# Kernel tuning notes

Hardware: AMD Instinct MI355X
Metric: run time of the kernel (lower is better)

## Reference

```python
import jax, jax.numpy as jnp
import numpy as np

N, D, R = 65536, 32, 128


def setup_inputs() -> dict:
    key = jax.random.key(0)
    k1, k2, k3, k4 = jax.random.split(key, 4)
    X = jax.random.normal(k1, (N, D), dtype=jnp.float32)
    a = jax.random.normal(k2, (R, D), dtype=jnp.float32)
    b = jax.random.uniform(k3, (R, D), dtype=jnp.float32)  # positive, like abs(randn)
    c = jax.random.normal(k4, (R, D + 1), dtype=jnp.float32)
    return {"X": X, "a": a, "b": b, "c": c}


def reference(X, a, b, c):
    # Gaussian membership per (sample, rule, dim): exp(-(x-a)^2 / (2*clamp(b,1e-8)^2))
    b_cl = jnp.clip(b, 1e-8)                      # [R, D]
    diff = X[:, None, :] - a[None, :, :]          # [N, R, D]
    mu = jnp.exp(-(diff * diff) / (2.0 * b_cl * b_cl))
    strengths = jnp.prod(mu, axis=2)              # [N, R] rule firing strengths
    strengths_sum = jnp.sum(strengths, axis=1, keepdims=True)
    normalized = strengths / (strengths_sum + 1e-8)
    # consequent: linear model per rule, X @ c[:, :-1].T + bias
    rule_out = X @ c[:, :-1].T + c[:, -1]         # [N, R]
    predictions = jnp.sum(normalized * rule_out, axis=1)  # [N]
    return (predictions, strengths, normalized)
```

## Files before the change

kernel.cpp:

```cpp
#include <hip/hip_runtime.h>

#define NS 65536
#define DD 32
#define RR 128
#define SPB 16
#define STR 132

__global__ __launch_bounds__(128, 4) void anfis_main(
    const float* __restrict__ X, const float* __restrict__ A,
    const float* __restrict__ B, const float* __restrict__ C,
    float* __restrict__ out_pred, float* __restrict__ out_str,
    float* __restrict__ out_norm)
{
    __shared__ float SBUF[SPB * STR];
    __shared__ float PBUF[SPB * STR];
    __shared__ float pS[SPB][8];
    __shared__ float pD[SPB][8];
    __shared__ float scale_lds[SPB];

    const int tid   = threadIdx.x;
    const int nbase = blockIdx.x * SPB;

    float w_[DD], naw_[DD], ck_[DD], bias;
    {
        const float4* av = (const float4*)(A + tid * DD);
        const float4* bv = (const float4*)(B + tid * DD);
        #pragma unroll
        for (int i = 0; i < 8; ++i) {
            float4 va = av[i], vb = bv[i];
            float w0 = 0.8493218003f * __builtin_amdgcn_rcpf(fmaxf(vb.x, 1e-8f));
            float w1 = 0.8493218003f * __builtin_amdgcn_rcpf(fmaxf(vb.y, 1e-8f));
            float w2 = 0.8493218003f * __builtin_amdgcn_rcpf(fmaxf(vb.z, 1e-8f));
            float w3 = 0.8493218003f * __builtin_amdgcn_rcpf(fmaxf(vb.w, 1e-8f));
            w_[4*i+0] = w0; naw_[4*i+0] = -va.x * w0;
            w_[4*i+1] = w1; naw_[4*i+1] = -va.y * w1;
            w_[4*i+2] = w2; naw_[4*i+2] = -va.z * w2;
            w_[4*i+3] = w3; naw_[4*i+3] = -va.w * w3;
        }
        #pragma unroll
        for (int d = 0; d < DD; ++d) ck_[d] = C[tid * (DD + 1) + d];
        bias = C[tid * (DD + 1) + DD];
    }

    const float* Xg = X + (size_t)nbase * DD;

    float xa[DD], xb[DD];
#define LOADX(arr, jj) { _Pragma("unroll") \
    for (int i = 0; i < DD; ++i) arr[i] = Xg[(jj) * DD + i]; }

#define COMPUTE(arr, jj) { \
    float s0 = 0.f, s1 = 0.f, s2 = 0.f, s3 = 0.f; \
    float r0 = bias, r1 = 0.f, r2 = 0.f, r3 = 0.f; \
    _Pragma("unroll") \
    for (int d = 0; d < DD; d += 4) { \
        float t0 = fmaf(arr[d+0], w_[d+0], naw_[d+0]); s0 = fmaf(t0, t0, s0); r0 = fmaf(arr[d+0], ck_[d+0], r0); \
        float t1 = fmaf(arr[d+1], w_[d+1], naw_[d+1]); s1 = fmaf(t1, t1, s1); r1 = fmaf(arr[d+1], ck_[d+1], r1); \
        float t2 = fmaf(arr[d+2], w_[d+2], naw_[d+2]); s2 = fmaf(t2, t2, s2); r2 = fmaf(arr[d+2], ck_[d+2], r2); \
        float t3 = fmaf(arr[d+3], w_[d+3], naw_[d+3]); s3 = fmaf(t3, t3, s3); r3 = fmaf(arr[d+3], ck_[d+3], r3); \
    } \
    float st = __builtin_amdgcn_exp2f(-((s0 + s1) + (s2 + s3))); \
    float ro = (r0 + r1) + (r2 + r3); \
    SBUF[(jj) * STR + tid] = st; \
    PBUF[(jj) * STR + tid] = st * ro; }

    LOADX(xa, 0)
    for (int j = 0; j < SPB; j += 2) {
        LOADX(xb, j + 1)
        COMPUTE(xa, j)
        if (j + 2 < SPB) LOADX(xa, j + 2)
        COMPUTE(xb, j + 1)
    }
#undef LOADX
#undef COMPUTE
    __syncthreads();

    {
        int s = tid >> 3, o = tid & 7;
        const float4* srow = (const float4*)&SBUF[s * STR + o * 16];
        const float4* prow = (const float4*)&PBUF[s * STR + o * 16];
        float ss = 0.f, dd = 0.f;
        #pragma unroll
        for (int k = 0; k < 4; ++k) {
            float4 v = srow[k]; ss += (v.x + v.y) + (v.z + v.w);
            float4 p = prow[k]; dd += (p.x + p.y) + (p.z + p.w);
        }
        pS[s][o] = ss; pD[s][o] = dd;
    }
    __syncthreads();
    if (tid < SPB) {
        float ss = 0.f, dd = 0.f;
        #pragma unroll
        for (int o = 0; o < 8; ++o) { ss += pS[tid][o]; dd += pD[tid][o]; }
        float sc = 1.0f / (ss + 1e-8f);
        out_pred[nbase + tid] = dd * sc;
        scale_lds[tid] = sc;
    }
    __syncthreads();

    #pragma unroll
    for (int it = 0; it < 4; ++it) {
        int f   = it * 128 + tid;
        int row = f >> 5;
        int col = f & 31;
        float4 v = *(const float4*)&SBUF[row * STR + col * 4];
        float sc = scale_lds[row];
        size_t base = ((size_t)(nbase + row)) * RR + col * 4;
        *(float4*)(out_str  + base) = v;
        *(float4*)(out_norm + base) = make_float4(v.x * sc, v.y * sc, v.z * sc, v.w * sc);
    }
}

extern "C" void kernel_launch(void* const* d_in, const int* in_sizes, int n_in,
                              void* d_out, int out_size, void* d_ws, size_t ws_size,
                              hipStream_t stream) {
    const float* X = (const float*)d_in[0];
    const float* A = (const float*)d_in[1];
    const float* B = (const float*)d_in[2];
    const float* C = (const float*)d_in[3];

    float* pred = (float*)d_out;
    float* str  = pred + NS;
    float* nrm  = str + (size_t)NS * RR;

    anfis_main<<<dim3(NS / SPB), dim3(128), 0, stream>>>(X, A, B, C, pred, str, nrm);
}
```

Before: 107.8 us.

## Process eight sample tiles per block with LDS-staged parameters and deferred stores

Each block now loops over eight 16-sample tiles instead of handling one. The per-rule weights, offsets and consequent coefficients are moved from registers into swizzled LDS arrays, and the loop is reordered so each thread accumulates 16 samples in registers while reading the block-uniform X rows. The strength and normalized outputs of the previous tile are written during the next tile's iteration, so global stores can overlap with compute; these stores are now per-thread scalar stores instead of float4 ones. This aims to spread parameter setup over more samples and hide store latency, at the cost of a lower occupancy target (launch bounds 2), more LDS use, and extra per-tile synchronisation.

```diff
diff --git a/kernel.cpp b/kernel.cpp
--- a/kernel.cpp
+++ b/kernel.cpp
@@ -3,110 +3,143 @@
 #define NS 65536
 #define DD 32
 #define RR 128
-#define SPB 16
-#define STR 132
+#define SPT 16
+#define TPB 8
+#define NBLK (NS / (SPT * TPB))
+#define TSTR 132
 
-__global__ __launch_bounds__(128, 4) void anfis_main(
+__global__ __launch_bounds__(128, 2) void anfis_main(
     const float* __restrict__ X, const float* __restrict__ A,
     const float* __restrict__ B, const float* __restrict__ C,
     float* __restrict__ out_pred, float* __restrict__ out_str,
     float* __restrict__ out_norm)
 {
-    __shared__ float SBUF[SPB * STR];
-    __shared__ float PBUF[SPB * STR];
-    __shared__ float pS[SPB][8];
-    __shared__ float pD[SPB][8];
-    __shared__ float scale_lds[SPB];
+    __shared__ float PW[RR * DD];
+    __shared__ float PN[RR * DD];
+    __shared__ float PK[RR * DD];
+    __shared__ float SB[SPT * TSTR];
+    __shared__ float PB[SPT * TSTR];
+    __shared__ float pS[SPT][8];
+    __shared__ float pD[SPT][8];
+    __shared__ float scl[SPT];
 
-    const int tid   = threadIdx.x;
-    const int nbase = blockIdx.x * SPB;
+    const int t = threadIdx.x;
 
-    float w_[DD], naw_[DD], ck_[DD], bias;
+    float bias;
     {
-        const float4* av = (const float4*)(A + tid * DD);
-        const float4* bv = (const float4*)(B + tid * DD);
+        const float4* av = (const float4*)(A + t * DD);
+        const float4* bv = (const float4*)(B + t * DD);
         #pragma unroll
-        for (int i = 0; i < 8; ++i) {
-            float4 va = av[i], vb = bv[i];
+        for (int c = 0; c < 8; ++c) {
+            float4 va = av[c], vb = bv[c];
             float w0 = 0.8493218003f * __builtin_amdgcn_rcpf(fmaxf(vb.x, 1e-8f));
             float w1 = 0.8493218003f * __builtin_amdgcn_rcpf(fmaxf(vb.y, 1e-8f));
             float w2 = 0.8493218003f * __builtin_amdgcn_rcpf(fmaxf(vb.z, 1e-8f));
             float w3 = 0.8493218003f * __builtin_amdgcn_rcpf(fmaxf(vb.w, 1e-8f));
-            w_[4*i+0] = w0; naw_[4*i+0] = -va.x * w0;
-            w_[4*i+1] = w1; naw_[4*i+1] = -va.y * w1;
-            w_[4*i+2] = w2; naw_[4*i+2] = -va.z * w2;
-            w_[4*i+3] = w3; naw_[4*i+3] = -va.w * w3;
+            int pc = t * DD + ((c + t) & 7) * 4;
+            *(float4*)&PW[pc] = make_float4(w0, w1, w2, w3);
+            *(float4*)&PN[pc] = make_float4(-va.x * w0, -va.y * w1, -va.z * w2, -va.w * w3);
+            *(float4*)&PK[pc] = make_float4(C[t*(DD+1)+4*c+0], C[t*(DD+1)+4*c+1],
+                                            C[t*(DD+1)+4*c+2], C[t*(DD+1)+4*c+3]);
         }
-        #pragma unroll
-        for (int d = 0; d < DD; ++d) ck_[d] = C[tid * (DD + 1) + d];
-        bias = C[tid * (DD + 1) + DD];
-    }
-
-    const float* Xg = X + (size_t)nbase * DD;
-
-    float xa[DD], xb[DD];
-#define LOADX(arr, jj) { _Pragma("unroll") \
-    for (int i = 0; i < DD; ++i) arr[i] = Xg[(jj) * DD + i]; }
-
-#define COMPUTE(arr, jj) { \
-    float s0 = 0.f, s1 = 0.f, s2 = 0.f, s3 = 0.f; \
-    float r0 = bias, r1 = 0.f, r2 = 0.f, r3 = 0.f; \
-    _Pragma("unroll") \
-    for (int d = 0; d < DD; d += 4) { \
-        float t0 = fmaf(arr[d+0], w_[d+0], naw_[d+0]); s0 = fmaf(t0, t0, s0); r0 = fmaf(arr[d+0], ck_[d+0], r0); \
-        float t1 = fmaf(arr[d+1], w_[d+1], naw_[d+1]); s1 = fmaf(t1, t1, s1); r1 = fmaf(arr[d+1], ck_[d+1], r1); \
-        float t2 = fmaf(arr[d+2], w_[d+2], naw_[d+2]); s2 = fmaf(t2, t2, s2); r2 = fmaf(arr[d+2], ck_[d+2], r2); \
-        float t3 = fmaf(arr[d+3], w_[d+3], naw_[d+3]); s3 = fmaf(t3, t3, s3); r3 = fmaf(arr[d+3], ck_[d+3], r3); \
-    } \
-    float st = __builtin_amdgcn_exp2f(-((s0 + s1) + (s2 + s3))); \
-    float ro = (r0 + r1) + (r2 + r3); \
-    SBUF[(jj) * STR + tid] = st; \
-    PBUF[(jj) * STR + tid] = st * ro; }
-
-    LOADX(xa, 0)
-    for (int j = 0; j < SPB; j += 2) {
-        LOADX(xb, j + 1)
-        COMPUTE(xa, j)
-        if (j + 2 < SPB) LOADX(xa, j + 2)
-        COMPUTE(xb, j + 1)
-    }
-#undef LOADX
-#undef COMPUTE
-    __syncthreads();
-
-    {
-        int s = tid >> 3, o = tid & 7;
-        const float4* srow = (const float4*)&SBUF[s * STR + o * 16];
-        const float4* prow = (const float4*)&PBUF[s * STR + o * 16];
-        float ss = 0.f, dd = 0.f;
-        #pragma unroll
-        for (int k = 0; k < 4; ++k) {
-            float4 v = srow[k]; ss += (v.x + v.y) + (v.z + v.w);
-            float4 p = prow[k]; dd += (p.x + p.y) + (p.z + p.w);
-        }
-        pS[s][o] = ss; pD[s][o] = dd;
-    }
-    __syncthreads();
-    if (tid < SPB) {
-        float ss = 0.f, dd = 0.f;
-        #pragma unroll
-        for (int o = 0; o < 8; ++o) { ss += pS[tid][o]; dd += pD[tid][o]; }
-        float sc = 1.0f / (ss + 1e-8f);
-        out_pred[nbase + tid] = dd * sc;
-        scale_lds[tid] = sc;
+        bias = C[t * (DD + 1) + DD];
     }
     __syncthreads();
 
-    #pragma unroll
-    for (int it = 0; it < 4; ++it) {
-        int f   = it * 128 + tid;
-        int row = f >> 5;
-        int col = f & 31;
-        float4 v = *(const float4*)&SBUF[row * STR + col * 4];
-        float sc = scale_lds[row];
-        size_t base = ((size_t)(nbase + row)) * RR + col * 4;
-        *(float4*)(out_str  + base) = v;
-        *(float4*)(out_norm + base) = make_float4(v.x * sc, v.y * sc, v.z * sc, v.w * sc);
+    const int nblock = blockIdx.x * (SPT * TPB);
+    float st_o[SPT];
+    int n_o = 0;
+
+    for (int tl = 0; tl < TPB; ++tl) {
+        const int n0 = nblock + tl * SPT;
+
+        if (tl > 0) {
+            float s4[SPT];
+            #pragma unroll
+            for (int q = 0; q < 4; ++q) {
+                float4 v = *(const float4*)&scl[q * 4];
+                s4[4*q+0] = v.x; s4[4*q+1] = v.y; s4[4*q+2] = v.z; s4[4*q+3] = v.w;
+            }
+            #pragma unroll
+            for (int s = 0; s < SPT; ++s) {
+                size_t base = (size_t)(n_o + s) * RR + t;
+                out_str[base]  = st_o[s];
+                out_norm[base] = st_o[s] * s4[s];
+            }
+        }
+
+        float as_[SPT], ar_[SPT];
+        #pragma unroll
+        for (int s = 0; s < SPT; ++s) { as_[s] = 0.0f; ar_[s] = bias; }
+
+        #pragma unroll
+        for (int c = 0; c < 8; ++c) {
+            const int pc = t * DD + ((c + t) & 7) * 4;
+            float4 w4 = *(const float4*)&PW[pc];
+            float4 n4 = *(const float4*)&PN[pc];
+            float4 k4 = *(const float4*)&PK[pc];
+            #pragma unroll
+            for (int s = 0; s < SPT; ++s) {
+                const float* xr = X + (size_t)(n0 + s) * DD + c * 4;
+                float x0 = xr[0], x1 = xr[1], x2 = xr[2], x3 = xr[3];
+                float t0 = fmaf(x0, w4.x, n4.x); as_[s] = fmaf(t0, t0, as_[s]); ar_[s] = fmaf(x0, k4.x, ar_[s]);
+                float t1 = fmaf(x1, w4.y, n4.y); as_[s] = fmaf(t1, t1, as_[s]); ar_[s] = fmaf(x1, k4.y, ar_[s]);
+                float t2 = fmaf(x2, w4.z, n4.z); as_[s] = fmaf(t2, t2, as_[s]); ar_[s] = fmaf(x2, k4.z, ar_[s]);
+                float t3 = fmaf(x3, w4.w, n4.w); as_[s] = fmaf(t3, t3, as_[s]); ar_[s] = fmaf(x3, k4.w, ar_[s]);
+            }
+        }
+
+        float st_[SPT];
+        #pragma unroll
+        for (int s = 0; s < SPT; ++s) {
+            float st = __builtin_amdgcn_exp2f(-as_[s]);
+            st_[s] = st;
+            SB[s * TSTR + t] = st;
+            PB[s * TSTR + t] = st * ar_[s];
+        }
+        __syncthreads();
+
+        {
+            int s = t >> 3, o = t & 7;
+            const float4* sr = (const float4*)&SB[s * TSTR + o * 16];
+            const float4* pr = (const float4*)&PB[s * TSTR + o * 16];
+            float ss = 0.f, dd = 0.f;
+            #pragma unroll
+            for (int k = 0; k < 4; ++k) {
+                float4 v = sr[k]; ss += (v.x + v.y) + (v.z + v.w);
+                float4 p = pr[k]; dd += (p.x + p.y) + (p.z + p.w);
+            }
+            pS[s][o] = ss; pD[s][o] = dd;
+        }
+        __syncthreads();
+        if (t < SPT) {
+            float ss = 0.f, dd = 0.f;
+            #pragma unroll
+            for (int o = 0; o < 8; ++o) { ss += pS[t][o]; dd += pD[t][o]; }
+            float sc = 1.0f / (ss + 1e-8f);
+            out_pred[n0 + t] = dd * sc;
+            scl[t] = sc;
+        }
+        __syncthreads();
+
+        #pragma unroll
+        for (int s = 0; s < SPT; ++s) st_o[s] = st_[s];
+        n_o = n0;
+    }
+
+    {
+        float s4[SPT];
+        #pragma unroll
+        for (int q = 0; q < 4; ++q) {
+            float4 v = *(const float4*)&scl[q * 4];
+            s4[4*q+0] = v.x; s4[4*q+1] = v.y; s4[4*q+2] = v.z; s4[4*q+3] = v.w;
+        }
+        #pragma unroll
+        for (int s = 0; s < SPT; ++s) {
+            size_t base = (size_t)(n_o + s) * RR + t;
+            out_str[base]  = st_o[s];
+            out_norm[base] = st_o[s] * s4[s];
+        }
     }
 }
 
@@ -122,5 +155,5 @@
     float* str  = pred + NS;
     float* nrm  = str + (size_t)NS * RR;
 
-    anfis_main<<<dim3(NS / SPB), dim3(128), 0, stream>>>(X, A, B, C, pred, str, nrm);
+    anfis_main<<<dim3(NBLK), dim3(128), 0, stream>>>(X, A, B, C, pred, str, nrm);
 }
```

Result: slower. 201.4 us (+86.8%).

## Precompute rule parameters in a prep kernel and stream them per chunk

Applied to the files above, without the earlier changes.

Adds a small pre-kernel that computes per-rule weights, offsets and consequent coefficients into workspace in a chunk-major float4 layout. The main kernel no longer keeps 96 per-rule parameters in registers. It loops over 8 dimension chunks, prefetching the next chunk's parameters, and keeps 16 per-sample accumulators instead. This cuts register pressure and removes the redundant per-block parameter setup. The cost is an extra kernel launch, scalar X reads with a different access pattern, and a serial loop-carried dependency on the accumulators.

```diff
diff --git a/kernel.cpp b/kernel.cpp
--- a/kernel.cpp
+++ b/kernel.cpp
@@ -6,9 +6,32 @@
 #define SPB 16
 #define STR 132
 
+__global__ void anfis_pre(const float* __restrict__ A, const float* __restrict__ B,
+                          const float* __restrict__ C, float4* __restrict__ PW,
+                          float4* __restrict__ PN, float4* __restrict__ PK,
+                          float* __restrict__ BIAS) {
+    int i = blockIdx.x * 256 + threadIdx.x;
+    if (i < RR * 8) {
+        int r = i >> 3, c = i & 7;
+        float4 va = *(const float4*)(A + r * DD + c * 4);
+        float4 vb = *(const float4*)(B + r * DD + c * 4);
+        float w0 = 0.8493218003f / fmaxf(vb.x, 1e-8f);
+        float w1 = 0.8493218003f / fmaxf(vb.y, 1e-8f);
+        float w2 = 0.8493218003f / fmaxf(vb.z, 1e-8f);
+        float w3 = 0.8493218003f / fmaxf(vb.w, 1e-8f);
+        int o = c * RR + r;
+        PW[o] = make_float4(w0, w1, w2, w3);
+        PN[o] = make_float4(-va.x * w0, -va.y * w1, -va.z * w2, -va.w * w3);
+        PK[o] = make_float4(C[r*(DD+1)+4*c+0], C[r*(DD+1)+4*c+1],
+                            C[r*(DD+1)+4*c+2], C[r*(DD+1)+4*c+3]);
+        if (c == 0) BIAS[r] = C[r * (DD + 1) + DD];
+    }
+}
+
 __global__ __launch_bounds__(128, 4) void anfis_main(
-    const float* __restrict__ X, const float* __restrict__ A,
-    const float* __restrict__ B, const float* __restrict__ C,
+    const float* __restrict__ X,
+    const float4* __restrict__ PW, const float4* __restrict__ PN,
+    const float4* __restrict__ PK, const float* __restrict__ BIAS,
     float* __restrict__ out_pred, float* __restrict__ out_str,
     float* __restrict__ out_norm)
 {
@@ -20,58 +43,36 @@
 
     const int tid   = threadIdx.x;
     const int nbase = blockIdx.x * SPB;
+    const float* Xg = X + (size_t)nbase * DD;
 
-    float w_[DD], naw_[DD], ck_[DD], bias;
-    {
-        const float4* av = (const float4*)(A + tid * DD);
-        const float4* bv = (const float4*)(B + tid * DD);
+    float as_[SPB], ar_[SPB];
+    const float bias = BIAS[tid];
+    #pragma unroll
+    for (int s = 0; s < SPB; ++s) { as_[s] = 0.0f; ar_[s] = bias; }
+
+    float4 w4 = PW[tid], n4 = PN[tid], k4 = PK[tid];
+    #pragma unroll 1
+    for (int c = 0; c < 8; ++c) {
+        const int cn = ((c + 1) & 7) * RR + tid;
+        float4 wn = PW[cn], nn = PN[cn], kn = PK[cn];
         #pragma unroll
-        for (int i = 0; i < 8; ++i) {
-            float4 va = av[i], vb = bv[i];
-            float w0 = 0.8493218003f * __builtin_amdgcn_rcpf(fmaxf(vb.x, 1e-8f));
-            float w1 = 0.8493218003f * __builtin_amdgcn_rcpf(fmaxf(vb.y, 1e-8f));
-            float w2 = 0.8493218003f * __builtin_amdgcn_rcpf(fmaxf(vb.z, 1e-8f));
-            float w3 = 0.8493218003f * __builtin_amdgcn_rcpf(fmaxf(vb.w, 1e-8f));
-            w_[4*i+0] = w0; naw_[4*i+0] = -va.x * w0;
-            w_[4*i+1] = w1; naw_[4*i+1] = -va.y * w1;
-            w_[4*i+2] = w2; naw_[4*i+2] = -va.z * w2;
-            w_[4*i+3] = w3; naw_[4*i+3] = -va.w * w3;
+        for (int s = 0; s < SPB; ++s) {
+            const float* xr = Xg + s * DD + c * 4;
+            float x0 = xr[0], x1 = xr[1], x2 = xr[2], x3 = xr[3];
+            float t0 = fmaf(x0, w4.x, n4.x); as_[s] = fmaf(t0, t0, as_[s]); ar_[s] = fmaf(x0, k4.x, ar_[s]);
+            float t1 = fmaf(x1, w4.y, n4.y); as_[s] = fmaf(t1, t1, as_[s]); ar_[s] = fmaf(x1, k4.y, ar_[s]);
+            float t2 = fmaf(x2, w4.z, n4.z); as_[s] = fmaf(t2, t2, as_[s]); ar_[s] = fmaf(x2, k4.z, ar_[s]);
+            float t3 = fmaf(x3, w4.w, n4.w); as_[s] = fmaf(t3, t3, as_[s]); ar_[s] = fmaf(x3, k4.w, ar_[s]);
         }
-        #pragma unroll
-        for (int d = 0; d < DD; ++d) ck_[d] = C[tid * (DD + 1) + d];
-        bias = C[tid * (DD + 1) + DD];
+        w4 = wn; n4 = nn; k4 = kn;
     }
 
-    const float* Xg = X + (size_t)nbase * DD;
-
-    float xa[DD], xb[DD];
-#define LOADX(arr, jj) { _Pragma("unroll") \
-    for (int i = 0; i < DD; ++i) arr[i] = Xg[(jj) * DD + i]; }
-
-#define COMPUTE(arr, jj) { \
-    float s0 = 0.f, s1 = 0.f, s2 = 0.f, s3 = 0.f; \
-    float r0 = bias, r1 = 0.f, r2 = 0.f, r3 = 0.f; \
-    _Pragma("unroll") \
-    for (int d = 0; d < DD; d += 4) { \
-        float t0 = fmaf(arr[d+0], w_[d+0], naw_[d+0]); s0 = fmaf(t0, t0, s0); r0 = fmaf(arr[d+0], ck_[d+0], r0); \
-        float t1 = fmaf(arr[d+1], w_[d+1], naw_[d+1]); s1 = fmaf(t1, t1, s1); r1 = fmaf(arr[d+1], ck_[d+1], r1); \
-        float t2 = fmaf(arr[d+2], w_[d+2], naw_[d+2]); s2 = fmaf(t2, t2, s2); r2 = fmaf(arr[d+2], ck_[d+2], r2); \
-        float t3 = fmaf(arr[d+3], w_[d+3], naw_[d+3]); s3 = fmaf(t3, t3, s3); r3 = fmaf(arr[d+3], ck_[d+3], r3); \
-    } \
-    float st = __builtin_amdgcn_exp2f(-((s0 + s1) + (s2 + s3))); \
-    float ro = (r0 + r1) + (r2 + r3); \
-    SBUF[(jj) * STR + tid] = st; \
-    PBUF[(jj) * STR + tid] = st * ro; }
-
-    LOADX(xa, 0)
-    for (int j = 0; j < SPB; j += 2) {
-        LOADX(xb, j + 1)
-        COMPUTE(xa, j)
-        if (j + 2 < SPB) LOADX(xa, j + 2)
-        COMPUTE(xb, j + 1)
+    #pragma unroll
+    for (int s = 0; s < SPB; ++s) {
+        float st = __builtin_amdgcn_exp2f(-as_[s]);
+        SBUF[s * STR + tid] = st;
+        PBUF[s * STR + tid] = st * ar_[s];
     }
-#undef LOADX
-#undef COMPUTE
     __syncthreads();
 
     {
@@ -118,9 +119,16 @@
     const float* B = (const float*)d_in[2];
     const float* C = (const float*)d_in[3];
 
+    float* wsf  = (float*)d_ws;
+    float4* PW  = (float4*)(wsf);
+    float4* PN  = (float4*)(wsf + RR * DD);
+    float4* PK  = (float4*)(wsf + 2 * RR * DD);
+    float* BIAS = wsf + 3 * RR * DD;
+
     float* pred = (float*)d_out;
     float* str  = pred + NS;
     float* nrm  = str + (size_t)NS * RR;
 
-    anfis_main<<<dim3(NS / SPB), dim3(128), 0, stream>>>(X, A, B, C, pred, str, nrm);
+    anfis_pre<<<dim3(4), dim3(256), 0, stream>>>(A, B, C, PW, PN, PK, BIAS);
+    anfis_main<<<dim3(NS / SPB), dim3(128), 0, stream>>>(X, PW, PN, PK, BIAS, pred, str, nrm);
 }
```

Result: no change. 107.6 us (-0.2%).
